# Kernel tuning notes

Measured on AMD Instinct MI355X. Metric: run time of the kernel, lower is better.

## Reference

```python
import jax, jax.numpy as jnp
import numpy as np


def setup_inputs() -> dict:
    key = jax.random.key(0)
    k1, k2, k3 = jax.random.split(key, 3)
    B, H, W, D, C, F = 2, 96, 128, 64, 32, 32
    images = jax.random.normal(k1, (B, H, W, D, C), dtype=jnp.float32)
    base_plane = jax.random.randint(k2, (B, H, W, 1), 0, 16, dtype=jnp.int32)
    kernel = jax.random.normal(k3, (3, 3, 3, C, F), dtype=jnp.float32) * 0.05
    default_value = jnp.zeros((), dtype=jnp.float32)
    return {"images": images, "base_plane": base_plane,
            "kernel": kernel, "default_value": default_value}


def _sparse_conv3d(images, base_plane, kernel, default_value):
    # images: [B,H,W,D,C] stored depth band per pixel, starting at base_plane
    # base_plane: [B,H,W,1] int, kernel: [KH,KW,KD,C,F]
    B, H, W, D, C = images.shape
    KH, KW, KD, _, F = kernel.shape
    ph, pw, pd = KH // 2, KW // 2, KD // 2
    bp = base_plane[..., 0]  # [B,H,W]

    # pad spatially once; out-of-image neighbors read default_value
    img_pad = jnp.pad(images, ((0, 0), (ph, ph), (pw, pw), (0, 0), (0, 0)))
    bp_pad = jnp.pad(bp, ((0, 0), (ph, ph), (pw, pw)))
    sp_valid_pad = jnp.pad(jnp.ones((H, W), dtype=bool),
                           ((ph, ph), (pw, pw)))

    d_grid = jnp.arange(D)[None, None, None, :]  # [1,1,1,D]
    out = jnp.zeros((B, H, W, D, F), dtype=images.dtype)

    for kh in range(KH):
        for kw in range(KW):
            img_s = img_pad[:, kh:kh + H, kw:kw + W]          # [B,H,W,D,C]
            bp_s = bp_pad[:, kh:kh + H, kw:kw + W]            # [B,H,W]
            sp_valid = sp_valid_pad[kh:kh + H, kw:kw + W]     # [H,W]
            for kd in range(KD):
                # neighbor stored-depth index = (d + bp) + (kd-pd) - bp_neighbor
                idx = d_grid + (bp - bp_s)[:, :, :, None] + (kd - pd)  # [B,H,W,D]
                valid = (idx >= 0) & (idx < D) & sp_valid[None, :, :, None]
                g = jnp.take_along_axis(
                    img_s, jnp.clip(idx, 0, D - 1)[..., None], axis=3)
                val = jnp.where(valid[..., None], g, default_value)
                out = out + jnp.einsum('bhwdc,cf->bhwdf', val,
                                       kernel[kh, kw, kd])
    return out


def reference(images, base_plane, kernel, default_value):
    return _sparse_conv3d(images, base_plane, kernel, default_value)
```

## Files before the change

### kernel.cpp

```cpp
#include <hip/hip_runtime.h>
#include <hip/hip_bf16.h>

#define Bn 2
#define Hn 96
#define Wn 128
#define Dn 64
#define Cn 32
#define Fn 32
#define TH 2
#define TW 8
#define CW (TW + 2)
#define NCOLS (4 * CW)
#define COLSZ (Dn * Cn)

typedef short bf16x8 __attribute__((ext_vector_type(8)));
typedef float f32x4  __attribute__((ext_vector_type(4)));

__device__ __forceinline__ ushort f2bf(float x) {
    __hip_bfloat16 h = __float2bfloat16(x);
    return *reinterpret_cast<ushort*>(&h);
}

__device__ __forceinline__ uint2 f4bf(float4 v) {
    uint2 r;
    asm("v_cvt_pk_bf16_f32 %0, %1, %2" : "=v"(r.x) : "v"(v.x), "v"(v.y));
    asm("v_cvt_pk_bf16_f32 %0, %1, %2" : "=v"(r.y) : "v"(v.z), "v"(v.w));
    return r;
}

__device__ __forceinline__ int swz_off(int r, int slot) {
    return r * 32 + ((slot ^ ((r >> 1) & 3)) << 3);
}

__global__ void prep_kT(const float* __restrict__ kern, ushort* __restrict__ kT) {
    const int e = blockIdx.x * 256 + threadIdx.x;
    if (e >= 30 * Cn * Fn) return;
    const int c  = e & 31;
    const int f  = (e >> 5) & 31;
    const int kk = e >> 10;
    kT[e] = (kk < 27) ? f2bf(kern[kk * (Cn * Fn) + c * Fn + f]) : (ushort)0;
}

__global__ __launch_bounds__(1024, 4) void sconv3d_mfma(
    const float*  __restrict__ img,
    const int*    __restrict__ bp,
    const float*  __restrict__ kern,
    const ushort* __restrict__ kT,
    const float*  __restrict__ dvp,
    float*        __restrict__ out)
{
    __shared__ ushort colS[NCOLS * COLSZ];

    const int xcd = blockIdx.x & 7;
    const int i   = blockIdx.x >> 3;
    const int ht  = i % (Hn / TH);
    const int q   = i / (Hn / TH);
    const int cI  = xcd * 4 + q;
    const int wt  = cI & 15;
    const int b   = cI >> 4;
    const int h0  = ht * TH;
    const int w0  = wt * TW;

    const int tid  = threadIdx.x;
    const int lane = tid & 63;
    const int wave = tid >> 6;
    const int ph   = wave >> 3;
    const int pw   = wave & 7;
    const int h    = h0 + ph;
    const int w    = w0 + pw;

    const int lrow = lane & 15;
    const int lgrp = lane >> 4;

    const float dv  = *dvp;
    const int   bpc = bp[(b * Hn + h) * Wn + w];

    int  sh[9];
    bool tv[9];
#pragma unroll
    for (int kh = 0; kh < 3; ++kh)
#pragma unroll
        for (int kw = 0; kw < 3; ++kw) {
            const int hh = h - 1 + kh;
            const int ww = w - 1 + kw;
            const bool v = (hh >= 0) && (hh < Hn) && (ww >= 0) && (ww < Wn);
            tv[kh * 3 + kw] = v;
            sh[kh * 3 + kw] = v ? (bpc - bp[(b * Hn + hh) * Wn + ww]) : 0;
        }

    {
        const int jbase = tid >> 9;
        const int sl    = tid & 511;
        const int swzT  = swz_off(sl >> 3, (sl >> 1) & 3) + (sl & 1) * 4;
        const bool wl_ok = !((w0 == 0) && (jbase == 0));
        const bool wr_ok = !((w0 == Wn - TW) && (jbase == 1));
        const float*  gbase = img + (size_t)((b * Hn + (h0 - 1)) * Wn + (w0 - 1) + jbase) * COLSZ + sl * 4;
        ushort*       lbase = colS + jbase * COLSZ + swzT;
#pragma unroll
        for (int it = 0; it < 20; ++it) {
            const int r  = (2 * it) / 10;
            const int cc = (2 * it) % 10;
            const int hh = h0 - 1 + r;
            const bool v = (hh >= 0) && (hh < Hn) &&
                           (cc == 0 ? wl_ok : (cc == 8 ? wr_ok : true));
            float4 x = make_float4(0.f, 0.f, 0.f, 0.f);
            if (v) x = *(const float4*)(gbase + (size_t)(r * Wn + cc) * COLSZ);
            const uint2 u = f4bf(x);
            *(uint2*)(lbase + 2 * it * COLSZ) = u;
        }
    }
    __syncthreads();

    f32x4 acc[4][2];
#pragma unroll
    for (int i2 = 0; i2 < 4; ++i2)
#pragma unroll
        for (int j2 = 0; j2 < 2; ++j2) acc[i2][j2] = (f32x4)0.f;

#pragma unroll
    for (int kh = 0; kh < 3; ++kh) {
#pragma unroll
        for (int kw = 0; kw < 3; ++kw) {
            const int t    = kh * 3 + kw;
            const int s    = sh[t];
            const int kkb  = tv[t] ? t * 3 : 27;
            const ushort* colp = &colS[((ph + kh) * CW + (pw + kw)) * COLSZ];
            bf16x8 bfr[3][2];
#pragma unroll
            for (int kd = 0; kd < 3; ++kd) {
                bfr[kd][0] = *(const bf16x8*)&kT[((kkb + kd) * Fn + lrow)      * Cn + lgrp * 8];
                bfr[kd][1] = *(const bf16x8*)&kT[((kkb + kd) * Fn + lrow + 16) * Cn + lgrp * 8];
            }
            __builtin_amdgcn_s_setprio(1);
#pragma unroll
            for (int kd = 0; kd < 3; ++kd) {
                const int i1 = 16 + lrow + s + kd - 1;
                const int o1 = swz_off(i1, lgrp);
                const bf16x8 a1 = *(const bf16x8*)&colp[o1];
                acc[1][0] = __builtin_amdgcn_mfma_f32_16x16x32_bf16(a1, bfr[kd][0], acc[1][0], 0, 0, 0);
                acc[1][1] = __builtin_amdgcn_mfma_f32_16x16x32_bf16(a1, bfr[kd][1], acc[1][1], 0, 0, 0);
                const bf16x8 a2 = *(const bf16x8*)&colp[o1 + 512];
                acc[2][0] = __builtin_amdgcn_mfma_f32_16x16x32_bf16(a2, bfr[kd][0], acc[2][0], 0, 0, 0);
                acc[2][1] = __builtin_amdgcn_mfma_f32_16x16x32_bf16(a2, bfr[kd][1], acc[2][1], 0, 0, 0);
                {
                    const bool vv = (i1 >= 16);
                    bf16x8 a0 = *(const bf16x8*)&colp[vv ? o1 - 512 : o1];
                    if (!vv) a0 = (bf16x8)0;
                    acc[0][0] = __builtin_amdgcn_mfma_f32_16x16x32_bf16(a0, bfr[kd][0], acc[0][0], 0, 0, 0);
                    acc[0][1] = __builtin_amdgcn_mfma_f32_16x16x32_bf16(a0, bfr[kd][1], acc[0][1], 0, 0, 0);
                }
                {
                    const bool vv = (i1 <= 31);
                    bf16x8 a3 = *(const bf16x8*)&colp[vv ? o1 + 1024 : o1];
                    if (!vv) a3 = (bf16x8)0;
                    acc[3][0] = __builtin_amdgcn_mfma_f32_16x16x32_bf16(a3, bfr[kd][0], acc[3][0], 0, 0, 0);
                    acc[3][1] = __builtin_amdgcn_mfma_f32_16x16x32_bf16(a3, bfr[kd][1], acc[3][1], 0, 0, 0);
                }
            }
            __builtin_amdgcn_s_setprio(0);
        }
    }

    if (dv != 0.0f) {
#pragma unroll
        for (int kh = 0; kh < 3; ++kh)
#pragma unroll
            for (int kw = 0; kw < 3; ++kw) {
                const bool sp = tv[kh * 3 + kw];
                const int  s  = sh[kh * 3 + kw];
                for (int kd = 0; kd < 3; ++kd) {
                    float ks0 = 0.f, ks1 = 0.f;
                    for (int c = 0; c < Cn; ++c) {
                        const float* kp = kern + (size_t)(((kh * 3 + kw) * 3 + kd) * Cn + c) * Fn;
                        ks0 += kp[lrow];
                        ks1 += kp[16 + lrow];
                    }
                    for (int dt = 0; dt < 4; ++dt)
                        for (int j = 0; j < 4; ++j) {
                            const int d   = dt * 16 + lgrp * 4 + j;
                            const int idx = d + s + kd - 1;
                            const bool valid = sp && (idx >= 0) && (idx < Dn);
                            if (!valid) { acc[dt][0][j] += dv * ks0; acc[dt][1][j] += dv * ks1; }
                        }
                }
            }
    }

    const size_t pixbase = ((size_t)(b * Hn + h) * Wn + w) * (Dn * Fn);
#pragma unroll
    for (int dt = 0; dt < 4; ++dt)
#pragma unroll
        for (int ft = 0; ft < 2; ++ft)
#pragma unroll
            for (int j = 0; j < 4; ++j) {
                const int d = dt * 16 + lgrp * 4 + j;
                const int f = ft * 16 + lrow;
                out[pixbase + d * Fn + f] = acc[dt][ft][j];
            }
}

extern "C" void kernel_launch(void* const* d_in, const int* in_sizes, int n_in,
                              void* d_out, int out_size, void* d_ws, size_t ws_size,
                              hipStream_t stream) {
    const float* img  = (const float*)d_in[0];
    const int*   bp   = (const int*)d_in[1];
    const float* kern = (const float*)d_in[2];
    const float* dvp  = (const float*)d_in[3];
    float* out = (float*)d_out;
    ushort* kT = (ushort*)d_ws;

    hipLaunchKernelGGL(prep_kT, dim3(120), dim3(256), 0, stream, kern, kT);

    const int nblk = Bn * (Hn / TH) * (Wn / TW);
    hipLaunchKernelGGL(sconv3d_mfma, dim3(nblk), dim3(1024), 0, stream,
                       img, bp, kern, kT, dvp, out);
}
```

Measured before the change: 176.0 us.

## Pre-convert image to swizzled bf16 and stage tiles with global_load_lds

Adds a separate pass that converts the whole fp32 image to bf16 in the LDS-swizzled layout in workspace, plus a zero buffer for out-of-bounds columns. The conv kernel then fills shared memory with direct global-to-LDS loads instead of loading fp32, converting and storing through registers. This halves the bytes read by the main kernel and removes the register round-trip. In exchange the extra pass reads the full fp32 image and writes a bf16 copy each call. The path only runs if the workspace is large enough, otherwise the old kernel is used.

Result: slower. 192.8 us (+9.5%).

```diff
diff --git a/kernel.cpp b/kernel.cpp
--- a/kernel.cpp
+++ b/kernel.cpp
@@ -13,6 +13,12 @@
 #define NCOLS (4 * CW)
 #define COLSZ (Dn * Cn)
 
+#define KT_OFF   0
+#define IMG_OFF  65536
+#define IMG_BYTES (Bn * Hn * Wn * Dn * Cn * 2)
+#define ZB_OFF   (IMG_OFF + IMG_BYTES)
+#define WS_NEED  (ZB_OFF + 4096)
+
 typedef short bf16x8 __attribute__((ext_vector_type(8)));
 typedef float f32x4  __attribute__((ext_vector_type(4)));
 
@@ -20,7 +26,6 @@
     __hip_bfloat16 h = __float2bfloat16(x);
     return *reinterpret_cast<ushort*>(&h);
 }
-
 __device__ __forceinline__ uint2 f4bf(float4 v) {
     uint2 r;
     asm("v_cvt_pk_bf16_f32 %0, %1, %2" : "=v"(r.x) : "v"(v.x), "v"(v.y));
@@ -41,8 +46,25 @@
     kT[e] = (kk < 27) ? f2bf(kern[kk * (Cn * Fn) + c * Fn + f]) : (ushort)0;
 }
 
-__global__ __launch_bounds__(1024, 4) void sconv3d_mfma(
-    const float*  __restrict__ img,
+__global__ __launch_bounds__(256) void cvt_img(const float* __restrict__ img,
+                                               ushort* __restrict__ imgbf,
+                                               ushort* __restrict__ zb) {
+    if (blockIdx.x == 0 && threadIdx.x < 256)
+        *(uint4*)&zb[threadIdx.x * 8] = make_uint4(0, 0, 0, 0);
+    const int nf4 = Bn * Hn * Wn * 512;
+    for (int e = blockIdx.x * 256 + threadIdx.x; e < nf4; e += 2048 * 256) {
+        const float4 v = *(const float4*)(img + (size_t)e * 4);
+        const int col = e >> 9;
+        const int sl  = e & 511;
+        const uint2 u = f4bf(v);
+        *(uint2*)&imgbf[(size_t)col * COLSZ
+                        + swz_off(sl >> 3, (sl >> 1) & 3) + (sl & 1) * 4] = u;
+    }
+}
+
+__global__ __launch_bounds__(1024, 4) void sconv3d_gl(
+    const ushort* __restrict__ imgbf,
+    const ushort* __restrict__ zb,
     const int*    __restrict__ bp,
     const float*  __restrict__ kern,
     const ushort* __restrict__ kT,
@@ -54,8 +76,8 @@
     const int xcd = blockIdx.x & 7;
     const int i   = blockIdx.x >> 3;
     const int ht  = i % (Hn / TH);
-    const int q   = i / (Hn / TH);
-    const int cI  = xcd * 4 + q;
+    const int q4  = i / (Hn / TH);
+    const int cI  = xcd * 4 + q4;
     const int wt  = cI & 15;
     const int b   = cI >> 4;
     const int h0  = ht * TH;
@@ -75,6 +97,28 @@
     const float dv  = *dvp;
     const int   bpc = bp[(b * Hn + h) * Wn + w];
 
+    {
+        const int e0 = wave * 10;
+#pragma unroll
+        for (int ii = 0; ii < 10; ++ii) {
+            const int e  = e0 + ii;
+            const int j  = e >> 2;
+            const int q  = e & 3;
+            const int r  = j / CW;
+            const int cc = j % CW;
+            const int hh = h0 - 1 + r;
+            const int ww = w0 - 1 + cc;
+            const bool v = (hh >= 0) && (hh < Hn) && (ww >= 0) && (ww < Wn);
+            const ushort* gpb = v ? (imgbf + (size_t)((b * Hn + hh) * Wn + ww) * COLSZ)
+                                  : zb;
+            const ushort* gp = gpb + q * 512 + lane * 8;
+            ushort* lp = colS + j * COLSZ + q * 512;
+            __builtin_amdgcn_global_load_lds(
+                (const __attribute__((address_space(1))) void*)gp,
+                (__attribute__((address_space(3))) void*)lp, 16, 0, 0);
+        }
+    }
+
     int  sh[9];
     bool tv[9];
 #pragma unroll
@@ -88,27 +132,6 @@
             sh[kh * 3 + kw] = v ? (bpc - bp[(b * Hn + hh) * Wn + ww]) : 0;
         }
 
-    {
-        const int jbase = tid >> 9;
-        const int sl    = tid & 511;
-        const int swzT  = swz_off(sl >> 3, (sl >> 1) & 3) + (sl & 1) * 4;
-        const bool wl_ok = !((w0 == 0) && (jbase == 0));
-        const bool wr_ok = !((w0 == Wn - TW) && (jbase == 1));
-        const float*  gbase = img + (size_t)((b * Hn + (h0 - 1)) * Wn + (w0 - 1) + jbase) * COLSZ + sl * 4;
-        ushort*       lbase = colS + jbase * COLSZ + swzT;
-#pragma unroll
-        for (int it = 0; it < 20; ++it) {
-            const int r  = (2 * it) / 10;
-            const int cc = (2 * it) % 10;
-            const int hh = h0 - 1 + r;
-            const bool v = (hh >= 0) && (hh < Hn) &&
-                           (cc == 0 ? wl_ok : (cc == 8 ? wr_ok : true));
-            float4 x = make_float4(0.f, 0.f, 0.f, 0.f);
-            if (v) x = *(const float4*)(gbase + (size_t)(r * Wn + cc) * COLSZ);
-            const uint2 u = f4bf(x);
-            *(uint2*)(lbase + 2 * it * COLSZ) = u;
-        }
-    }
     __syncthreads();
 
     f32x4 acc[4][2];
@@ -199,6 +222,146 @@
             }
 }
 
+__global__ __launch_bounds__(1024, 4) void sconv3d_mfma(
+    const float*  __restrict__ img,
+    const int*    __restrict__ bp,
+    const float*  __restrict__ kern,
+    const ushort* __restrict__ kT,
+    const float*  __restrict__ dvp,
+    float*        __restrict__ out)
+{
+    __shared__ ushort colS[NCOLS * COLSZ];
+    const int xcd = blockIdx.x & 7;
+    const int i   = blockIdx.x >> 3;
+    const int ht  = i % (Hn / TH);
+    const int q   = i / (Hn / TH);
+    const int cI  = xcd * 4 + q;
+    const int wt  = cI & 15;
+    const int b   = cI >> 4;
+    const int h0  = ht * TH;
+    const int w0  = wt * TW;
+    const int tid  = threadIdx.x;
+    const int lane = tid & 63;
+    const int wave = tid >> 6;
+    const int ph   = wave >> 3;
+    const int pw   = wave & 7;
+    const int h    = h0 + ph;
+    const int w    = w0 + pw;
+    const int lrow = lane & 15;
+    const int lgrp = lane >> 4;
+    const float dv  = *dvp;
+    const int   bpc = bp[(b * Hn + h) * Wn + w];
+    int  sh[9]; bool tv[9];
+#pragma unroll
+    for (int kh = 0; kh < 3; ++kh)
+#pragma unroll
+        for (int kw = 0; kw < 3; ++kw) {
+            const int hh = h - 1 + kh, ww = w - 1 + kw;
+            const bool v = (hh >= 0) && (hh < Hn) && (ww >= 0) && (ww < Wn);
+            tv[kh * 3 + kw] = v;
+            sh[kh * 3 + kw] = v ? (bpc - bp[(b * Hn + hh) * Wn + ww]) : 0;
+        }
+    {
+        const int jbase = tid >> 9;
+        const int sl    = tid & 511;
+        const int swzT  = swz_off(sl >> 3, (sl >> 1) & 3) + (sl & 1) * 4;
+        const bool wl_ok = !((w0 == 0) && (jbase == 0));
+        const bool wr_ok = !((w0 == Wn - TW) && (jbase == 1));
+        const float* gbase = img + (size_t)((b * Hn + (h0 - 1)) * Wn + (w0 - 1) + jbase) * COLSZ + sl * 4;
+        ushort*      lbase = colS + jbase * COLSZ + swzT;
+#pragma unroll
+        for (int it = 0; it < 20; ++it) {
+            const int r  = (2 * it) / 10;
+            const int cc = (2 * it) % 10;
+            const int hh = h0 - 1 + r;
+            const bool v = (hh >= 0) && (hh < Hn) &&
+                           (cc == 0 ? wl_ok : (cc == 8 ? wr_ok : true));
+            float4 x = make_float4(0.f, 0.f, 0.f, 0.f);
+            if (v) x = *(const float4*)(gbase + (size_t)(r * Wn + cc) * COLSZ);
+            const uint2 u = f4bf(x);
+            *(uint2*)(lbase + 2 * it * COLSZ) = u;
+        }
+    }
+    __syncthreads();
+    f32x4 acc[4][2];
+#pragma unroll
+    for (int i2 = 0; i2 < 4; ++i2)
+#pragma unroll
+        for (int j2 = 0; j2 < 2; ++j2) acc[i2][j2] = (f32x4)0.f;
+#pragma unroll
+    for (int kh = 0; kh < 3; ++kh)
+#pragma unroll
+        for (int kw = 0; kw < 3; ++kw) {
+            const int t    = kh * 3 + kw;
+            const int s    = sh[t];
+            const int kkb  = tv[t] ? t * 3 : 27;
+            const ushort* colp = &colS[((ph + kh) * CW + (pw + kw)) * COLSZ];
+            bf16x8 bfr[3][2];
+#pragma unroll
+            for (int kd = 0; kd < 3; ++kd) {
+                bfr[kd][0] = *(const bf16x8*)&kT[((kkb + kd) * Fn + lrow)      * Cn + lgrp * 8];
+                bfr[kd][1] = *(const bf16x8*)&kT[((kkb + kd) * Fn + lrow + 16) * Cn + lgrp * 8];
+            }
+            __builtin_amdgcn_s_setprio(1);
+#pragma unroll
+            for (int kd = 0; kd < 3; ++kd) {
+                const int i1 = 16 + lrow + s + kd - 1;
+                const int o1 = swz_off(i1, lgrp);
+                const bf16x8 a1 = *(const bf16x8*)&colp[o1];
+                acc[1][0] = __builtin_amdgcn_mfma_f32_16x16x32_bf16(a1, bfr[kd][0], acc[1][0], 0, 0, 0);
+                acc[1][1] = __builtin_amdgcn_mfma_f32_16x16x32_bf16(a1, bfr[kd][1], acc[1][1], 0, 0, 0);
+                const bf16x8 a2 = *(const bf16x8*)&colp[o1 + 512];
+                acc[2][0] = __builtin_amdgcn_mfma_f32_16x16x32_bf16(a2, bfr[kd][0], acc[2][0], 0, 0, 0);
+                acc[2][1] = __builtin_amdgcn_mfma_f32_16x16x32_bf16(a2, bfr[kd][1], acc[2][1], 0, 0, 0);
+                { const bool vv = (i1 >= 16);
+                  bf16x8 a0 = *(const bf16x8*)&colp[vv ? o1 - 512 : o1];
+                  if (!vv) a0 = (bf16x8)0;
+                  acc[0][0] = __builtin_amdgcn_mfma_f32_16x16x32_bf16(a0, bfr[kd][0], acc[0][0], 0, 0, 0);
+                  acc[0][1] = __builtin_amdgcn_mfma_f32_16x16x32_bf16(a0, bfr[kd][1], acc[0][1], 0, 0, 0); }
+                { const bool vv = (i1 <= 31);
+                  bf16x8 a3 = *(const bf16x8*)&colp[vv ? o1 + 1024 : o1];
+                  if (!vv) a3 = (bf16x8)0;
+                  acc[3][0] = __builtin_amdgcn_mfma_f32_16x16x32_bf16(a3, bfr[kd][0], acc[3][0], 0, 0, 0);
+                  acc[3][1] = __builtin_amdgcn_mfma_f32_16x16x32_bf16(a3, bfr[kd][1], acc[3][1], 0, 0, 0); }
+            }
+            __builtin_amdgcn_s_setprio(0);
+        }
+    if (dv != 0.0f) {
+#pragma unroll
+        for (int kh = 0; kh < 3; ++kh)
+#pragma unroll
+            for (int kw = 0; kw < 3; ++kw) {
+                const bool sp = tv[kh * 3 + kw];
+                const int  s  = sh[kh * 3 + kw];
+                for (int kd = 0; kd < 3; ++kd) {
+                    float ks0 = 0.f, ks1 = 0.f;
+                    for (int c = 0; c < Cn; ++c) {
+                        const float* kp = kern + (size_t)(((kh * 3 + kw) * 3 + kd) * Cn + c) * Fn;
+                        ks0 += kp[lrow]; ks1 += kp[16 + lrow];
+                    }
+                    for (int dt = 0; dt < 4; ++dt)
+                        for (int j = 0; j < 4; ++j) {
+                            const int d   = dt * 16 + lgrp * 4 + j;
+                            const int idx = d + s + kd - 1;
+                            const bool valid = sp && (idx >= 0) && (idx < Dn);
+                            if (!valid) { acc[dt][0][j] += dv * ks0; acc[dt][1][j] += dv * ks1; }
+                        }
+                }
+            }
+    }
+    const size_t pixbase = ((size_t)(b * Hn + h) * Wn + w) * (Dn * Fn);
+#pragma unroll
+    for (int dt = 0; dt < 4; ++dt)
+#pragma unroll
+        for (int ft = 0; ft < 2; ++ft)
+#pragma unroll
+            for (int j = 0; j < 4; ++j) {
+                const int d = dt * 16 + lgrp * 4 + j;
+                const int f = ft * 16 + lrow;
+                out[pixbase + d * Fn + f] = acc[dt][ft][j];
+            }
+}
+
 extern "C" void kernel_launch(void* const* d_in, const int* in_sizes, int n_in,
                               void* d_out, int out_size, void* d_ws, size_t ws_size,
                               hipStream_t stream) {
@@ -207,11 +370,20 @@
     const float* kern = (const float*)d_in[2];
     const float* dvp  = (const float*)d_in[3];
     float* out = (float*)d_out;
-    ushort* kT = (ushort*)d_ws;
-
+
+    ushort* kT = (ushort*)((char*)d_ws + KT_OFF);
     hipLaunchKernelGGL(prep_kT, dim3(120), dim3(256), 0, stream, kern, kT);
 
     const int nblk = Bn * (Hn / TH) * (Wn / TW);
-    hipLaunchKernelGGL(sconv3d_mfma, dim3(nblk), dim3(1024), 0, stream,
-                       img, bp, kern, kT, dvp, out);
-}
+
+    if (ws_size >= (size_t)WS_NEED) {
+        ushort* imgbf = (ushort*)((char*)d_ws + IMG_OFF);
+        ushort* zb    = (ushort*)((char*)d_ws + ZB_OFF);
+        hipLaunchKernelGGL(cvt_img, dim3(2048), dim3(256), 0, stream, img, imgbf, zb);
+        hipLaunchKernelGGL(sconv3d_gl, dim3(nblk), dim3(1024), 0, stream,
+                           imgbf, zb, bp, kern, kT, dvp, out);
+    } else {
+        hipLaunchKernelGGL(sconv3d_mfma, dim3(nblk), dim3(1024), 0, stream,
+                           img, bp, kern, kT, dvp, out);
+    }
+}
```
